# Performance work log

Measured on AMD Instinct MI355X. Metric: run time of the kernel, lower is better.

The kernel has to match this reference:

```python
import jax, jax.numpy as jnp
import numpy as np

N_CELLS = 200_000
N_FACES = 400_000
N_POINTS = 200_000
E_CF = 800_000
E_FP = 800_000
E_PP = 1_200_000
IN_C, IN_F, HID, OUT = 8, 8, 64, 128


def setup_inputs() -> dict:
    key = jax.random.key(0)
    ks = jax.random.split(key, 18)
    return {
        "x_centers": jax.random.normal(ks[0], (N_CELLS, IN_C), jnp.float32),
        "x_face": jax.random.normal(ks[1], (N_FACES, IN_F), jnp.float32),
        "W_cf": jax.random.normal(ks[2], (IN_C, HID), jnp.float32) * 0.1,
        "b_cf": jax.random.normal(ks[3], (HID,), jnp.float32) * 0.1,
        "W_fp": jax.random.normal(ks[4], (HID + IN_F, OUT), jnp.float32) * 0.1,
        "b_fp": jax.random.normal(ks[5], (OUT,), jnp.float32) * 0.1,
        "W_pp": jax.random.normal(ks[6], (OUT, OUT), jnp.float32) * 0.1,
        "W_pp_root": jax.random.normal(ks[7], (OUT, OUT), jnp.float32) * 0.1,
        "b_pp": jax.random.normal(ks[8], (OUT,), jnp.float32) * 0.1,
        "ea_cf": jax.random.uniform(ks[9], (E_CF,), jnp.float32),
        "ea_fp": jax.random.uniform(ks[10], (E_FP,), jnp.float32),
        "ea_pp": jax.random.uniform(ks[11], (E_PP,), jnp.float32),
        "src_cf": jax.random.randint(ks[12], (E_CF,), 0, N_CELLS, jnp.int32),
        "dst_cf": jax.random.randint(ks[13], (E_CF,), 0, N_FACES, jnp.int32),
        "src_fp": jax.random.randint(ks[14], (E_FP,), 0, N_FACES, jnp.int32),
        "dst_fp": jax.random.randint(ks[15], (E_FP,), 0, N_POINTS, jnp.int32),
        "src_pp": jax.random.randint(ks[16], (E_PP,), 0, N_POINTS, jnp.int32),
        "dst_pp": jax.random.randint(ks[17], (E_PP,), 0, N_POINTS, jnp.int32),
    }


def _graph_conv(x, W, b, src, dst, ea, n_dst):
    # transform-then-gather (small in-dim GEMM first), weight by edge_attr, scatter-sum
    h = x @ W                                   # [n_src, out]
    msg = h[src] * ea[:, None]                  # [E, out]
    return jax.ops.segment_sum(msg, dst, num_segments=n_dst) + b


def reference(x_centers, x_face, W_cf, b_cf, W_fp, b_fp, W_pp, W_pp_root, b_pp,
              ea_cf, ea_fp, ea_pp, src_cf, dst_cf, src_fp, dst_fp, src_pp, dst_pp):
    # layerCenterFace: cells -> faces
    y_face = _graph_conv(x_centers, W_cf, b_cf, src_cf, dst_cf, ea_cf, N_FACES)
    # concat learned face features with raw face features
    x = jnp.concatenate([y_face, x_face], axis=-1)          # [N_FACES, 72]
    # layerFacePoint: faces -> points
    y_pt = _graph_conv(x, W_fp, b_fp, src_fp, dst_fp, ea_fp, N_POINTS)
    # layerPointPoint: points -> points with root/self term
    msg = (y_pt @ W_pp)[src_pp] * ea_pp[:, None]            # [E_PP, 128]
    agg = jax.ops.segment_sum(msg, dst_pp, num_segments=N_POINTS)
    return y_pt @ W_pp_root + agg + b_pp                    # [N_POINTS, 128]
```

## Files before the change

kernel.cpp:

```cpp
#include <hip/hip_runtime.h>
#include <hip/hip_bf16.h>

#define N_CELLS  200000
#define N_FACES  400000
#define N_POINTS 200000
#define E_CF     800000
#define E_FP     800000
#define E_PP     1200000
#define CAP_CF   16
#define CAP_FP   24
#define CAP_PP   32
#define OVF_CAP  4096

typedef __attribute__((ext_vector_type(4))) float f32x4;

__device__ __forceinline__ float bf2f(unsigned short u) {
    union { unsigned int i; float f; } v; v.i = ((unsigned int)u) << 16; return v.f;
}
__device__ __forceinline__ unsigned short f2bf(float f) {
    __hip_bfloat16 h = __float2bfloat16(f);
    return *reinterpret_cast<unsigned short*>(&h);
}
__device__ __forceinline__ int2 ldnt2(const int2* p) {
    long long v = __builtin_nontemporal_load((const long long*)p);
    int2 r; r.x = (int)(v & 0xffffffffLL); r.y = (int)(v >> 32); return r;
}

__device__ __forceinline__ void fill_fixed(const int* __restrict__ src,
                                           const int* __restrict__ dst,
                                           const float* __restrict__ ea,
                                           int nE, int rlo, int rhi, int cap,
                                           int tid0, int stride,
                                           int* __restrict__ cnt,
                                           int2* __restrict__ pe,
                                           int* __restrict__ ovfn,
                                           int4* __restrict__ ovf) {
    for (int e = tid0; e < nE; e += stride) {
        int4 d4 = *(const int4*)(dst + e);
        int4 s4 = *(const int4*)(src + e);
        float4 w4 = *(const float4*)(ea + e);
        int dd[4] = {d4.x, d4.y, d4.z, d4.w};
        int ss[4] = {s4.x, s4.y, s4.z, s4.w};
        float ww[4] = {w4.x, w4.y, w4.z, w4.w};
#pragma unroll
        for (int i = 0; i < 4; ++i) {
            int d = dd[i];
            if (d >= rlo && d < rhi) {
                int t = atomicAdd(&cnt[d], 1);
                if (t < cap)
                    pe[(size_t)d * cap + t] = make_int2(ss[i], __float_as_int(ww[i]));
                else {
                    int g = atomicAdd(ovfn, 1);
                    if (g < OVF_CAP) ovf[g] = make_int4(d, ss[i], __float_as_int(ww[i]), 0);
                }
            }
        }
    }
}

__global__ __launch_bounds__(256) void k_fillA(const int* __restrict__ src_cf,
                                               const int* __restrict__ dst_cf,
                                               const float* __restrict__ ea_cf,
                                               int* __restrict__ cnt_cf,
                                               int2* __restrict__ pe_cf,
                                               const int* __restrict__ src_pp,
                                               const int* __restrict__ dst_pp,
                                               const float* __restrict__ ea_pp,
                                               int* __restrict__ cnt_pp,
                                               int2* __restrict__ pe_pp,
                                               int* __restrict__ ovfn,
                                               int4* __restrict__ ovf_cf,
                                               int4* __restrict__ ovf_pp,
                                               const float* __restrict__ W_cf,
                                               const float* __restrict__ b_cf,
                                               const float* __restrict__ W_fp,
                                               const float* __restrict__ b_fp,
                                               const float* __restrict__ W_rt,
                                               const float* __restrict__ W_pp,
                                               const float* __restrict__ b_pp,
                                               float* __restrict__ WALL) {
    __shared__ float WcfS[512];
    __shared__ float bcfS[64];
    __shared__ float WtL[18 * 128];
    int b = blockIdx.x;
    if (b < 512) {
        int p = b & 3;
        int blk = b >> 2;
        int rlo = p * 100000, rhi = rlo + 100000;
        int tid0 = (blk * 256 + (int)threadIdx.x) * 4;
        fill_fixed(src_cf, dst_cf, ea_cf, E_CF, rlo, rhi, CAP_CF,
                   tid0, 128 * 256 * 4, cnt_cf, pe_cf, ovfn, ovf_cf);
    } else if (b < 1024) {
        int bb = b - 512;
        int p = bb & 3;
        int blk = bb >> 2;
        int rlo = p * 50000, rhi = rlo + 50000;
        int tid0 = (blk * 256 + (int)threadIdx.x) * 4;
        fill_fixed(src_pp, dst_pp, ea_pp, E_PP, rlo, rhi, CAP_PP,
                   tid0, 128 * 256 * 4, cnt_pp, pe_pp, ovfn + 2, ovf_pp);
    } else {
        for (int i = threadIdx.x; i < 512; i += 256) WcfS[i] = W_cf[i];
        if (threadIdx.x < 64) bcfS[threadIdx.x] = b_cf[threadIdx.x];
        __syncthreads();
        int t = threadIdx.x;
        int j = t & 127;
        if (t < 128) {
            float accW[8] = {};
            float accb = 0.f;
            for (int m = 0; m < 64; ++m) {
                float wf = W_fp[m * 128 + j];
#pragma unroll
                for (int k = 0; k < 8; ++k) accW[k] += WcfS[k * 64 + m] * wf;
                accb += bcfS[m] * wf;
            }
#pragma unroll
            for (int k = 0; k < 8; ++k) WtL[k * 128 + j] = accW[k];
            WtL[16 * 128 + j] = accb;
        } else {
#pragma unroll
            for (int k = 0; k < 8; ++k) WtL[(8 + k) * 128 + j] = W_fp[(64 + k) * 128 + j];
            WtL[17 * 128 + j] = b_fp[j];
        }
        __syncthreads();
        for (int i = threadIdx.x; i < 36 * 128; i += 256) {
            int r = i >> 7, jj = i & 127;
            float acc;
            if (r < 17) {
                acc = 0.f;
                for (int k = 0; k < 128; ++k) acc += WtL[r * 128 + k] * W_rt[k * 128 + jj];
            } else if (r < 34) {
                acc = 0.f;
                for (int k = 0; k < 128; ++k) acc += WtL[(r - 17) * 128 + k] * W_pp[k * 128 + jj];
            } else if (r == 34) {
                acc = 0.f;
                for (int k = 0; k < 128; ++k) acc += WtL[17 * 128 + k] * W_pp[k * 128 + jj];
            } else {
                acc = b_pp[jj];
                for (int k = 0; k < 128; ++k) acc += WtL[17 * 128 + k] * W_rt[k * 128 + jj];
            }
            WALL[i] = acc;
        }
    }
}

__global__ __launch_bounds__(256) void k_fillB(const int* __restrict__ src_fp,
                                               const int* __restrict__ dst_fp,
                                               const float* __restrict__ ea_fp,
                                               int* __restrict__ cnt_fp,
                                               int2* __restrict__ pe_fp,
                                               int* __restrict__ ovfn,
                                               int4* __restrict__ ovf_fp,
                                               const float* __restrict__ xc,
                                               const int* __restrict__ cnt_cf,
                                               const int2* __restrict__ pe_cf,
                                               const int* __restrict__ ovfn_cf,
                                               const int4* __restrict__ ovf_cf,
                                               const float* __restrict__ x_face,
                                               float* __restrict__ aggcx) {
    int b = blockIdx.x;
    if (b < 512) {
        int p = b & 3;
        int blk = b >> 2;
        int rlo = p * 50000, rhi = rlo + 50000;
        int tid0 = (blk * 256 + (int)threadIdx.x) * 4;
        fill_fixed(src_fp, dst_fp, ea_fp, E_FP, rlo, rhi, CAP_FP,
                   tid0, 128 * 256 * 4, cnt_fp, pe_fp, ovfn + 1, ovf_fp);
        return;
    }
    int r = (b - 512) * 256 + threadIdx.x;
    if (r >= N_FACES) return;
    int n = cnt_cf[r]; if (n > CAP_CF) n = CAP_CF;
    const int2* prow = pe_cf + (size_t)r * CAP_CF;
    float a[8] = {};
    int e = 0;
    for (; e + 1 < n; e += 2) {
        int2 q0 = prow[e], q1 = prow[e + 1];
        float w0 = __int_as_float(q0.y), w1 = __int_as_float(q1.y);
        const float* p0 = xc + (size_t)q0.x * 8;
        const float* p1 = xc + (size_t)q1.x * 8;
        float4 u0 = *(const float4*)p0, u1 = *(const float4*)(p0 + 4);
        float4 v0 = *(const float4*)p1, v1 = *(const float4*)(p1 + 4);
        a[0] += w0 * u0.x + w1 * v0.x; a[1] += w0 * u0.y + w1 * v0.y;
        a[2] += w0 * u0.z + w1 * v0.z; a[3] += w0 * u0.w + w1 * v0.w;
        a[4] += w0 * u1.x + w1 * v1.x; a[5] += w0 * u1.y + w1 * v1.y;
        a[6] += w0 * u1.z + w1 * v1.z; a[7] += w0 * u1.w + w1 * v1.w;
    }
    if (e < n) {
        int2 q0 = prow[e];
        float w0 = __int_as_float(q0.y);
        const float* p0 = xc + (size_t)q0.x * 8;
        float4 u0 = *(const float4*)p0, u1 = *(const float4*)(p0 + 4);
        a[0] += w0 * u0.x; a[1] += w0 * u0.y; a[2] += w0 * u0.z; a[3] += w0 * u0.w;
        a[4] += w0 * u1.x; a[5] += w0 * u1.y; a[6] += w0 * u1.z; a[7] += w0 * u1.w;
    }
    int no = *ovfn_cf;
    if (no > 0) {
        if (no > OVF_CAP) no = OVF_CAP;
        for (int i = 0; i < no; ++i) {
            int4 o = ovf_cf[i];
            if (o.x == r) {
                float w0 = __int_as_float(o.z);
                const float* p0 = xc + (size_t)o.y * 8;
#pragma unroll
                for (int k = 0; k < 8; ++k) a[k] += w0 * p0[k];
            }
        }
    }
    float4 xf0 = *(const float4*)(x_face + (size_t)r * 8);
    float4 xf1 = *(const float4*)(x_face + (size_t)r * 8 + 4);
    float4* o4 = (float4*)(aggcx + (size_t)r * 16);
    o4[0] = make_float4(a[0], a[1], a[2], a[3]);
    o4[1] = make_float4(a[4], a[5], a[6], a[7]);
    o4[2] = xf0;
    o4[3] = xf1;
}

__global__ __launch_bounds__(256) void k_g16(const float* __restrict__ aggcx,
                                             const int* __restrict__ cnt,
                                             const int2* __restrict__ pe,
                                             const int* __restrict__ ovfn,
                                             const int4* __restrict__ ovf,
                                             unsigned short* __restrict__ a16b,
                                             float* __restrict__ s_fp) {
    const int grp = threadIdx.x >> 4;
    const int l = threadIdx.x & 15;
    const int row = blockIdx.x * 16 + grp;
    int n = cnt[row]; if (n > CAP_FP) n = CAP_FP;
    const int2* prow = pe + (size_t)row * CAP_FP;
    float acc = 0.f, s = 0.f;
    int e = 0;
    for (; e + 1 < n; e += 2) {
        int2 q0 = ldnt2(prow + e);
        int2 q1 = ldnt2(prow + e + 1);
        float w0 = __int_as_float(q0.y), w1 = __int_as_float(q1.y);
        acc += w0 * aggcx[(size_t)q0.x * 16 + l] + w1 * aggcx[(size_t)q1.x * 16 + l];
        s += w0 + w1;
    }
    if (e < n) {
        int2 q0 = ldnt2(prow + e);
        float w0 = __int_as_float(q0.y);
        acc += w0 * aggcx[(size_t)q0.x * 16 + l];
        s += w0;
    }
    int no = *ovfn;
    if (no > 0) {
        if (no > OVF_CAP) no = OVF_CAP;
        for (int i = 0; i < no; ++i) {
            int4 o = ovf[i];
            if (o.x == row) {
                float w0 = __int_as_float(o.z);
                acc += w0 * aggcx[(size_t)o.y * 16 + l];
                s += w0;
            }
        }
    }
    a16b[(size_t)row * 16 + l] = f2bf(acc);
    if (l == 0) s_fp[row] = s;
}

__global__ __launch_bounds__(256) void k_fin(const unsigned short* __restrict__ a16b,
                                             const float* __restrict__ s_fp,
                                             const int* __restrict__ cnt,
                                             const int2* __restrict__ pe,
                                             const int* __restrict__ ovfn,
                                             const int4* __restrict__ ovf,
                                             const float* __restrict__ WALL,
                                             float* __restrict__ out) {
    __shared__ float W36[36 * 128];
    for (int i = threadIdx.x; i < 36 * 128; i += 256) W36[i] = WALL[i];
    __syncthreads();
    const int grp = threadIdx.x >> 4;
    const int l = threadIdx.x & 15;
    const int row = blockIdx.x * 16 + grp;
    int n = cnt[row]; if (n > CAP_PP) n = CAP_PP;
    const int2* prow = pe + (size_t)row * CAP_PP;
    float App = 0.f, Spp = 0.f, Tpp = 0.f;
    int e = 0;
    for (; e + 1 < n; e += 2) {
        int2 q0 = ldnt2(prow + e);
        int2 q1 = ldnt2(prow + e + 1);
        float w0 = __int_as_float(q0.y), w1 = __int_as_float(q1.y);
        App += w0 * bf2f(a16b[(size_t)q0.x * 16 + l]) + w1 * bf2f(a16b[(size_t)q1.x * 16 + l]);
        Spp += w0 * s_fp[q0.x] + w1 * s_fp[q1.x];
        Tpp += w0 + w1;
    }
    if (e < n) {
        int2 q0 = ldnt2(prow + e);
        float w0 = __int_as_float(q0.y);
        App += w0 * bf2f(a16b[(size_t)q0.x * 16 + l]);
        Spp += w0 * s_fp[q0.x];
        Tpp += w0;
    }
    int no = *ovfn;
    if (no > 0) {
        if (no > OVF_CAP) no = OVF_CAP;
        for (int i = 0; i < no; ++i) {
            int4 o = ovf[i];
            if (o.x == row) {
                float w0 = __int_as_float(o.z);
                App += w0 * bf2f(a16b[(size_t)o.y * 16 + l]);
                Spp += w0 * s_fp[o.y];
                Tpp += w0;
            }
        }
    }
    float aown = bf2f(a16b[(size_t)row * 16 + l]);
    float sown = s_fp[row];
    const int jc = l * 8;
    float o[8];
    {
        const float4* bb = (const float4*)(W36 + 35 * 128 + jc);
        const float4* sr = (const float4*)(W36 + 16 * 128 + jc);
        const float4* Sr = (const float4*)(W36 + 33 * 128 + jc);
        const float4* Tr = (const float4*)(W36 + 34 * 128 + jc);
        float4 b0 = bb[0], b1 = bb[1];
        float4 s0 = sr[0], s1 = sr[1];
        float4 S0 = Sr[0], S1 = Sr[1];
        float4 T0 = Tr[0], T1 = Tr[1];
        o[0] = b0.x + sown * s0.x + Spp * S0.x + Tpp * T0.x;
        o[1] = b0.y + sown * s0.y + Spp * S0.y + Tpp * T0.y;
        o[2] = b0.z + sown * s0.z + Spp * S0.z + Tpp * T0.z;
        o[3] = b0.w + sown * s0.w + Spp * S0.w + Tpp * T0.w;
        o[4] = b1.x + sown * s1.x + Spp * S1.x + Tpp * T1.x;
        o[5] = b1.y + sown * s1.y + Spp * S1.y + Tpp * T1.y;
        o[6] = b1.z + sown * s1.z + Spp * S1.z + Tpp * T1.z;
        o[7] = b1.w + sown * s1.w + Spp * S1.w + Tpp * T1.w;
    }
#pragma unroll
    for (int r = 0; r < 16; ++r) {
        float av = __shfl(aown, r, 16);
        const float4* wr = (const float4*)(W36 + r * 128 + jc);
        float4 w0 = wr[0], w1 = wr[1];
        o[0] += av * w0.x; o[1] += av * w0.y; o[2] += av * w0.z; o[3] += av * w0.w;
        o[4] += av * w1.x; o[5] += av * w1.y; o[6] += av * w1.z; o[7] += av * w1.w;
    }
#pragma unroll
    for (int r = 0; r < 16; ++r) {
        float av = __shfl(App, r, 16);
        const float4* wr = (const float4*)(W36 + (17 + r) * 128 + jc);
        float4 w0 = wr[0], w1 = wr[1];
        o[0] += av * w0.x; o[1] += av * w0.y; o[2] += av * w0.z; o[3] += av * w0.w;
        o[4] += av * w1.x; o[5] += av * w1.y; o[6] += av * w1.z; o[7] += av * w1.w;
    }
    float* op = out + (size_t)row * 128 + jc;
    f32x4 v0 = {o[0], o[1], o[2], o[3]};
    f32x4 v1 = {o[4], o[5], o[6], o[7]};
    __builtin_nontemporal_store(v0, (f32x4*)op);
    __builtin_nontemporal_store(v1, (f32x4*)(op + 4));
}

extern "C" void kernel_launch(void* const* d_in, const int* in_sizes, int n_in,
                              void* d_out, int out_size, void* d_ws, size_t ws_size,
                              hipStream_t stream) {
    const float* x_centers = (const float*)d_in[0];
    const float* x_face    = (const float*)d_in[1];
    const float* W_cf      = (const float*)d_in[2];
    const float* b_cf      = (const float*)d_in[3];
    const float* W_fp      = (const float*)d_in[4];
    const float* b_fp      = (const float*)d_in[5];
    const float* W_pp      = (const float*)d_in[6];
    const float* W_rt      = (const float*)d_in[7];
    const float* b_pp      = (const float*)d_in[8];
    const float* ea_cf     = (const float*)d_in[9];
    const float* ea_fp     = (const float*)d_in[10];
    const float* ea_pp     = (const float*)d_in[11];
    const int* src_cf      = (const int*)d_in[12];
    const int* dst_cf      = (const int*)d_in[13];
    const int* src_fp      = (const int*)d_in[14];
    const int* dst_fp      = (const int*)d_in[15];
    const int* src_pp      = (const int*)d_in[16];
    const int* dst_pp      = (const int*)d_in[17];
    float* out = (float*)d_out;

    char* ws = (char*)d_ws;
    float* aggcx           = (float*)(ws + 0);
    unsigned short* a16b   = (unsigned short*)(ws + 28000000);
    float* s_fp            = (float*)(ws + 36000000);
    float* WALL            = (float*)(ws + 44000000);
    int2* pe_fp            = (int2*)(ws + 50000000);
    int2* pe_cf            = (int2*)(ws + 90000000);
    int2* pe_pp            = (int2*)(ws + 145000000);
    int*  cnt_cf           = (int*)(ws + 280000000);
    int*  cnt_fp           = (int*)(ws + 281600000);
    int*  cnt_pp           = (int*)(ws + 282400000);
    int*  ovfn             = (int*)(ws + 283200000);
    int4* ovf_cf           = (int4*)(ws + 284000000);
    int4* ovf_fp           = (int4*)(ws + 284100000);
    int4* ovf_pp           = (int4*)(ws + 284200000);

    (void)hipMemsetAsync(cnt_cf, 0, 3200016, stream);
    k_fillA<<<1025, 256, 0, stream>>>(src_cf, dst_cf, ea_cf, cnt_cf, pe_cf,
                                      src_pp, dst_pp, ea_pp, cnt_pp, pe_pp,
                                      ovfn, ovf_cf, ovf_pp,
                                      W_cf, b_cf, W_fp, b_fp, W_rt, W_pp, b_pp,
                                      WALL);
    k_fillB<<<512 + 1563, 256, 0, stream>>>(src_fp, dst_fp, ea_fp, cnt_fp, pe_fp,
                                            ovfn, ovf_fp,
                                            x_centers, cnt_cf, pe_cf, ovfn, ovf_cf,
                                            x_face, aggcx);
    k_g16<<<12500, 256, 0, stream>>>(aggcx, cnt_fp, pe_fp, ovfn + 1, ovf_fp, a16b, s_fp);
    k_fin<<<12500, 256, 0, stream>>>(a16b, s_fp, cnt_pp, pe_pp, ovfn + 2, ovf_pp, WALL, out);
}
```

Before: 333.9 us.

## Split point-point bucket fill across two kernels and interleave output columns

The point-point edge bucketing is divided so k_fillA handles destination rows below 130000 and k_fillB handles the rest, alongside the face-point fill and the cell aggregation. This balances fill work between the first two launches. The final kernel also switches from each lane owning 8 contiguous output columns with float4 loads and stores to lanes owning columns strided by 16. That makes a 16-lane group write a contiguous 64-byte span per store, at the cost of scalar weight loads and scalar stores.

```diff
diff --git a/kernel.cpp b/kernel.cpp
--- a/kernel.cpp
+++ b/kernel.cpp
@@ -11,6 +11,7 @@
 #define CAP_FP   24
 #define CAP_PP   32
 #define OVF_CAP  4096
+#define PP_SPLIT 130000
 
 typedef __attribute__((ext_vector_type(4))) float f32x4;
 
@@ -94,7 +95,7 @@
         int bb = b - 512;
         int p = bb & 3;
         int blk = bb >> 2;
-        int rlo = p * 50000, rhi = rlo + 50000;
+        int rlo = p * 32500, rhi = rlo + 32500;
         int tid0 = (blk * 256 + (int)threadIdx.x) * 4;
         fill_fixed(src_pp, dst_pp, ea_pp, E_PP, rlo, rhi, CAP_PP,
                    tid0, 128 * 256 * 4, cnt_pp, pe_pp, ovfn + 2, ovf_pp);
@@ -148,8 +149,14 @@
                                                const float* __restrict__ ea_fp,
                                                int* __restrict__ cnt_fp,
                                                int2* __restrict__ pe_fp,
+                                               const int* __restrict__ src_pp,
+                                               const int* __restrict__ dst_pp,
+                                               const float* __restrict__ ea_pp,
+                                               int* __restrict__ cnt_pp,
+                                               int2* __restrict__ pe_pp,
                                                int* __restrict__ ovfn,
                                                int4* __restrict__ ovf_fp,
+                                               int4* __restrict__ ovf_pp,
                                                const float* __restrict__ xc,
                                                const int* __restrict__ cnt_cf,
                                                const int2* __restrict__ pe_cf,
@@ -167,7 +174,17 @@
                    tid0, 128 * 256 * 4, cnt_fp, pe_fp, ovfn + 1, ovf_fp);
         return;
     }
-    int r = (b - 512) * 256 + threadIdx.x;
+    if (b < 1024) {
+        int bb = b - 512;
+        int p = bb & 3;
+        int blk = bb >> 2;
+        int rlo = PP_SPLIT + p * 17500, rhi = rlo + 17500;
+        int tid0 = (blk * 256 + (int)threadIdx.x) * 4;
+        fill_fixed(src_pp, dst_pp, ea_pp, E_PP, rlo, rhi, CAP_PP,
+                   tid0, 128 * 256 * 4, cnt_pp, pe_pp, ovfn + 2, ovf_pp);
+        return;
+    }
+    int r = (b - 1024) * 256 + threadIdx.x;
     if (r >= N_FACES) return;
     int n = cnt_cf[r]; if (n > CAP_CF) n = CAP_CF;
     const int2* prow = pe_cf + (size_t)r * CAP_CF;
@@ -306,47 +323,31 @@
     }
     float aown = bf2f(a16b[(size_t)row * 16 + l]);
     float sown = s_fp[row];
-    const int jc = l * 8;
     float o[8];
-    {
-        const float4* bb = (const float4*)(W36 + 35 * 128 + jc);
-        const float4* sr = (const float4*)(W36 + 16 * 128 + jc);
-        const float4* Sr = (const float4*)(W36 + 33 * 128 + jc);
-        const float4* Tr = (const float4*)(W36 + 34 * 128 + jc);
-        float4 b0 = bb[0], b1 = bb[1];
-        float4 s0 = sr[0], s1 = sr[1];
-        float4 S0 = Sr[0], S1 = Sr[1];
-        float4 T0 = Tr[0], T1 = Tr[1];
-        o[0] = b0.x + sown * s0.x + Spp * S0.x + Tpp * T0.x;
-        o[1] = b0.y + sown * s0.y + Spp * S0.y + Tpp * T0.y;
-        o[2] = b0.z + sown * s0.z + Spp * S0.z + Tpp * T0.z;
-        o[3] = b0.w + sown * s0.w + Spp * S0.w + Tpp * T0.w;
-        o[4] = b1.x + sown * s1.x + Spp * S1.x + Tpp * T1.x;
-        o[5] = b1.y + sown * s1.y + Spp * S1.y + Tpp * T1.y;
-        o[6] = b1.z + sown * s1.z + Spp * S1.z + Tpp * T1.z;
-        o[7] = b1.w + sown * s1.w + Spp * S1.w + Tpp * T1.w;
+#pragma unroll
+    for (int k = 0; k < 8; ++k) {
+        int c = 16 * k + l;
+        o[k] = W36[35 * 128 + c] + sown * W36[16 * 128 + c]
+             + Spp * W36[33 * 128 + c] + Tpp * W36[34 * 128 + c];
     }
 #pragma unroll
     for (int r = 0; r < 16; ++r) {
         float av = __shfl(aown, r, 16);
-        const float4* wr = (const float4*)(W36 + r * 128 + jc);
-        float4 w0 = wr[0], w1 = wr[1];
-        o[0] += av * w0.x; o[1] += av * w0.y; o[2] += av * w0.z; o[3] += av * w0.w;
-        o[4] += av * w1.x; o[5] += av * w1.y; o[6] += av * w1.z; o[7] += av * w1.w;
+        const float* wr = W36 + r * 128 + l;
+#pragma unroll
+        for (int k = 0; k < 8; ++k) o[k] += av * wr[16 * k];
     }
 #pragma unroll
     for (int r = 0; r < 16; ++r) {
         float av = __shfl(App, r, 16);
-        const float4* wr = (const float4*)(W36 + (17 + r) * 128 + jc);
-        float4 w0 = wr[0], w1 = wr[1];
-        o[0] += av * w0.x; o[1] += av * w0.y; o[2] += av * w0.z; o[3] += av * w0.w;
-        o[4] += av * w1.x; o[5] += av * w1.y; o[6] += av * w1.z; o[7] += av * w1.w;
-    }
-    float* op = out + (size_t)row * 128 + jc;
-    f32x4 v0 = {o[0], o[1], o[2], o[3]};
-    f32x4 v1 = {o[4], o[5], o[6], o[7]};
-    __builtin_nontemporal_store(v0, (f32x4*)op);
-    __builtin_nontemporal_store(v1, (f32x4*)(op + 4));
+        const float* wr = W36 + (17 + r) * 128 + l;
+#pragma unroll
+        for (int k = 0; k < 8; ++k) o[k] += av * wr[16 * k];
+    }
+    float* op = out + (size_t)row * 128 + l;
+#pragma unroll
+    for (int k = 0; k < 8; ++k)
+        __builtin_nontemporal_store(o[k], op + 16 * k);
 }
 
 extern "C" void kernel_launch(void* const* d_in, const int* in_sizes, int n_in,
@@ -394,10 +395,11 @@
                                       ovfn, ovf_cf, ovf_pp,
                                       W_cf, b_cf, W_fp, b_fp, W_rt, W_pp, b_pp,
                                       WALL);
-    k_fillB<<<512 + 1563, 256, 0, stream>>>(src_fp, dst_fp, ea_fp, cnt_fp, pe_fp,
-                                            ovfn, ovf_fp,
-                                            x_centers, cnt_cf, pe_cf, ovfn, ovf_cf,
-                                            x_face, aggcx);
+    k_fillB<<<1024 + 1563, 256, 0, stream>>>(src_fp, dst_fp, ea_fp, cnt_fp, pe_fp,
+                                             src_pp, dst_pp, ea_pp, cnt_pp, pe_pp,
+                                             ovfn, ovf_fp, ovf_pp,
+                                             x_centers, cnt_cf, pe_cf, ovfn, ovf_cf,
+                                             x_face, aggcx);
     k_g16<<<12500, 256, 0, stream>>>(aggcx, cnt_fp, pe_fp, ovfn + 1, ovf_fp, a16b, s_fp);
     k_fin<<<12500, 256, 0, stream>>>(a16b, s_fp, cnt_pp, pe_pp, ovfn + 2, ovf_pp, WALL, out);
 }
```

Result: no change. 328.1 us (median of 2 runs) (-1.7%).
